# Kernel tuning notes

Hardware: AMD Instinct MI355X
Metric: run time of the kernel (lower is better)

The kernel has to match this reference:

```python
import jax, jax.numpy as jnp
import numpy as np

TEMPERATURE = 0.1
USE_RANKS = True
USE_SCORES = True
RANK_WEIGHT = 0.1
SCORE_WEIGHT = 0.01
NUM_GROUPS = 1024  # question_ids in [0, NUM_GROUPS)
BATCH = 4096
DIM = 1024


def setup_inputs() -> dict:
    key = jax.random.key(0)
    k1, k2, k3, k4, k5 = jax.random.split(key, 5)
    q_embeddings = jax.random.normal(k1, (BATCH, DIM), dtype=jnp.float32)
    a_embeddings = jax.random.normal(k2, (BATCH, DIM), dtype=jnp.float32)
    question_ids = jax.random.randint(k3, (BATCH,), 0, NUM_GROUPS, dtype=jnp.int32)
    ranks = jax.random.uniform(k4, (BATCH,), dtype=jnp.float32) * 8.0  # ordinal-ish ranks
    scores = jax.random.uniform(k5, (BATCH,), dtype=jnp.float32)
    return {
        "q_embeddings": q_embeddings,
        "a_embeddings": a_embeddings,
        "question_ids": question_ids,
        "ranks": ranks,
        "scores": scores,
    }


def _positive_weights(question_ids, ranks, scores):
    """Per-sample positive weight, normalized to sum to 1 within each question group."""
    w = jnp.ones_like(ranks)
    if USE_RANKS:
        w = w * jnp.exp(-RANK_WEIGHT * ranks)
    if USE_SCORES:
        gmax = jax.ops.segment_max(scores, question_ids, num_segments=NUM_GROUPS)
        gmin = jax.ops.segment_min(scores, question_ids, num_segments=NUM_GROUPS)
        denom = gmax[question_ids] - gmin[question_ids]
        norm = jnp.where(denom > 0, (scores - gmin[question_ids]) / jnp.where(denom > 0, denom, 1.0), 0.0)
        w = w * jnp.exp(SCORE_WEIGHT * norm)
    wsum = jax.ops.segment_sum(w, question_ids, num_segments=NUM_GROUPS)[question_ids]
    gsize = jax.ops.segment_sum(jnp.ones_like(w), question_ids, num_segments=NUM_GROUPS)[question_ids]
    w = jnp.where(wsum > 0, w / jnp.where(wsum > 0, wsum, 1.0), 1.0 / gsize)
    return w


def reference(q_embeddings, a_embeddings, question_ids, ranks, scores):
    B = q_embeddings.shape[0]
    # [B, B] similarity, one fused batched log-softmax over rows
    similarity = jnp.matmul(q_embeddings, a_embeddings.T) / TEMPERATURE
    log_probs = jax.nn.log_softmax(similarity, axis=1)
    # same-group mask: sample j is a positive for row i iff same question id
    same = (question_ids[:, None] == question_ids[None, :])
    w = _positive_weights(question_ids, ranks, scores)  # [B], group-normalized
    # loss_i = -sum_{j in group(i)} w_j * log_probs[i, j]; total averaged over batch
    per_row = -jnp.sum(jnp.where(same, w[None, :] * log_probs, 0.0), axis=1)
    loss = jnp.sum(per_row) / B
    # accuracy: argmax of each row lands inside the row's group
    pred = jnp.argmax(similarity, axis=1)
    acc = jnp.mean((question_ids[pred] == question_ids).astype(jnp.float32))
    return loss, acc
```

## Files before the change

kernel.cpp:

```cpp
#include <hip/hip_runtime.h>
#include <hip/hip_bf16.h>
#include <math.h>

#define BATCH   4096
#define DIM     1024
#define NGROUPS 1024
#define INV_T   10.0f
#define RANK_W  0.1f
#define SCORE_W 0.01f

#define BI 256
#define BJ 256
#define KC 32
#define NSTAGE (DIM/KC)
#define NFRAG_Q (BI/16)
#define NFRAG   (BI/16 + BJ/16)
#define FRAG_ELEMS 512

typedef float  floatx4 __attribute__((ext_vector_type(4)));
typedef __bf16 bf16x8  __attribute__((ext_vector_type(8)));
typedef __bf16 bf16x4  __attribute__((ext_vector_type(4)));

#define ASYNC_COPY16(gptr, lptr)                                              \
    __builtin_amdgcn_global_load_lds(                                         \
        (const __attribute__((address_space(1))) void*)(gptr),                \
        (__attribute__((address_space(3))) void*)(lptr), 16, 0, 0)


__global__ __launch_bounds__(256) void prep_kernel(
    const float* __restrict__ Q, const float* __restrict__ A,
    __bf16* __restrict__ Qp, __bf16* __restrict__ Ap,
    const int* __restrict__ qid, const float* __restrict__ ranks,
    const float* __restrict__ scores, float* __restrict__ w)
{
    const int tid = threadIdx.x;

    if (blockIdx.x >= NGROUPS) {
        __shared__ __bf16 stile[4][16 * 40];
        const int wid  = tid >> 6, lane = tid & 63;
        const int fid  = (blockIdx.x - NGROUPS) * 4 + wid;
        const int m    = fid >> 13;
        const int loc  = fid & 8191;
        const int p    = loc >> 9;
        const int t    = (loc >> 4) & 31;
        const int fi   = loc & 15;

        const float* src = (m ? A : Q);
        __bf16*      dst = (m ? Ap : Qp) + (size_t)loc * FRAG_ELEMS;

        const int r  = lane >> 2;
        const int kq = lane & 3;
        const size_t base = (size_t)(p * 256 + fi * 16 + r) * DIM + t * KC;
        const float4 v1 = *(const float4*)(src + base + kq * 4);
        const float4 v2 = *(const float4*)(src + base + 16 + kq * 4);
        bf16x4 b1, b2;
        b1[0] = (__bf16)v1.x; b1[1] = (__bf16)v1.y;
        b1[2] = (__bf16)v1.z; b1[3] = (__bf16)v1.w;
        b2[0] = (__bf16)v2.x; b2[1] = (__bf16)v2.y;
        b2[2] = (__bf16)v2.z; b2[3] = (__bf16)v2.w;

        *(bf16x4*)&stile[wid][r * 40 + kq * 4]      = b1;
        *(bf16x4*)&stile[wid][r * 40 + 16 + kq * 4] = b2;
        bf16x8 g = *(const bf16x8*)&stile[wid][(lane & 15) * 40 + (lane >> 4) * 8];
        *(bf16x8*)&dst[lane * 8] = g;
        return;
    }

    const int g = blockIdx.x, lane = tid & 63, wv = tid >> 6;
    __shared__ float rmax[4], rmin[4], rsum[4];

    float gmax = -INFINITY, gmin = INFINITY;
    for (int j = tid; j < BATCH; j += 256) {
        if (qid[j] == g) {
            float s = scores[j];
            gmax = fmaxf(gmax, s);
            gmin = fminf(gmin, s);
        }
    }
    #pragma unroll
    for (int d = 1; d < 64; d <<= 1) {
        gmax = fmaxf(gmax, __shfl_xor(gmax, d, 64));
        gmin = fminf(gmin, __shfl_xor(gmin, d, 64));
    }
    if (lane == 0) { rmax[wv] = gmax; rmin[wv] = gmin; }
    __syncthreads();
    gmax = fmaxf(fmaxf(rmax[0], rmax[1]), fmaxf(rmax[2], rmax[3]));
    gmin = fminf(fminf(rmin[0], rmin[1]), fminf(rmin[2], rmin[3]));
    const float denom     = gmax - gmin;
    const float inv_denom = (denom > 0.f) ? 1.f / denom : 0.f;

    float lsum = 0.f;
    for (int j = tid; j < BATCH; j += 256) {
        if (qid[j] == g) {
            float norm = (scores[j] - gmin) * inv_denom;
            float u = __expf(-RANK_W * ranks[j] + SCORE_W * norm);
            w[j] = u;
            lsum += u;
        }
    }
    #pragma unroll
    for (int d = 1; d < 64; d <<= 1) lsum += __shfl_xor(lsum, d, 64);
    if (lane == 0) rsum[wv] = lsum;
    __syncthreads();
    const float wsum = rsum[0] + rsum[1] + rsum[2] + rsum[3];
    const float inv  = (wsum > 0.f) ? 1.f / wsum : 0.f;
    for (int j = tid; j < BATCH; j += 256) {
        if (qid[j] == g) w[j] *= inv;
    }
}

__global__ __launch_bounds__(1024, 4) void fused_simloss_kernel(
    const __bf16* __restrict__ Qp, const __bf16* __restrict__ Ap,
    const int* __restrict__ qid, const float* __restrict__ w,
    float* __restrict__ Pm, float* __restrict__ Pl, float* __restrict__ Ps,
    float* __restrict__ Pbv, int* __restrict__ Pbi)
{
    __shared__ __bf16 sbuf[2][NFRAG * FRAG_ELEMS];

    const int bid = blockIdx.x;
    const int ib = bid >> 4, jb = bid & 15;
    const int i0 = ib * BI, j0 = jb * BJ;

    const int tid = threadIdx.x, wid = tid >> 6, lane = tid & 63;
    const int wm = wid >> 2, wn = wid & 3;
    const int quad = lane >> 4, l16 = lane & 15;

    floatx4 acc[4][4];
    #pragma unroll
    for (int m = 0; m < 4; ++m)
        #pragma unroll
        for (int n = 0; n < 4; ++n)
            #pragma unroll
            for (int c = 0; c < 4; ++c) acc[m][n][c] = 0.f;

    const __bf16* src[2];
    #pragma unroll
    for (int c = 0; c < 2; ++c) {
        const int f = wid * 2 + c;
        src[c] = (f < NFRAG_Q)
               ? Qp + ((size_t)(ib * NSTAGE * 16 + f)) * FRAG_ELEMS + lane * 8
               : Ap + ((size_t)(jb * NSTAGE * 16 + (f - NFRAG_Q))) * FRAG_ELEMS + lane * 8;
    }

    #define STAGE(buf, t)                                                     \
        do {                                                                  \
            _Pragma("unroll")                                                 \
            for (int c = 0; c < 2; ++c)                                       \
                ASYNC_COPY16(src[c] + (size_t)(t) * (16 * FRAG_ELEMS),        \
                             &sbuf[buf][(wid * 2 + c) * FRAG_ELEMS]);         \
        } while (0)

    STAGE(0, 0);

    for (int t = 0; t < NSTAGE; ++t) {
        __syncthreads();
        if (t + 1 < NSTAGE) STAGE((t + 1) & 1, t + 1);

        const __bf16* cur = sbuf[t & 1];
        bf16x8 qf[4], af[4];
        #pragma unroll
        for (int mf = 0; mf < 4; ++mf)
            qf[mf] = *(const bf16x8*)&cur[(wm * 4 + mf) * FRAG_ELEMS + lane * 8];
        #pragma unroll
        for (int nf = 0; nf < 4; ++nf)
            af[nf] = *(const bf16x8*)&cur[(NFRAG_Q + wn * 4 + nf) * FRAG_ELEMS + lane * 8];
        #pragma unroll
        for (int nf = 0; nf < 4; ++nf)
            #pragma unroll
            for (int mf = 0; mf < 4; ++mf)
                acc[mf][nf] = __builtin_amdgcn_mfma_f32_16x16x32_bf16(
                    qf[mf], af[nf], acc[mf][nf], 0, 0, 0);
    }
    #undef STAGE

    int cq[4]; float cw[4];
    #pragma unroll
    for (int n = 0; n < 4; ++n) {
        int col = j0 + wn * 64 + n * 16 + l16;
        cq[n] = qid[col];
        cw[n] = w[col];
    }
    const int slice = jb * 4 + wn;

    #pragma unroll
    for (int m = 0; m < 4; ++m) {
        #pragma unroll
        for (int reg = 0; reg < 4; ++reg) {
            const int row = i0 + wm * 64 + m * 16 + quad * 4 + reg;
            const int rq  = qid[row];

            float v[4];
            #pragma unroll
            for (int n = 0; n < 4; ++n) v[n] = acc[m][n][reg] * INV_T;

            float lm = fmaxf(fmaxf(v[0], v[1]), fmaxf(v[2], v[3]));
            float ll = __expf(v[0] - lm) + __expf(v[1] - lm) +
                       __expf(v[2] - lm) + __expf(v[3] - lm);
            float ls = 0.f;
            #pragma unroll
            for (int n = 0; n < 4; ++n) ls += (cq[n] == rq) ? cw[n] * v[n] : 0.f;

            float bv = v[0];
            int   bi = j0 + wn * 64 + l16;
            #pragma unroll
            for (int n = 1; n < 4; ++n) {
                int c = j0 + wn * 64 + n * 16 + l16;
                if (v[n] > bv) { bv = v[n]; bi = c; }
            }

            #pragma unroll
            for (int d = 1; d < 16; d <<= 1) {
                float om  = __shfl_xor(lm, d, 64);
                float ol  = __shfl_xor(ll, d, 64);
                float os  = __shfl_xor(ls, d, 64);
                float obv = __shfl_xor(bv, d, 64);
                int   obi = __shfl_xor(bi, d, 64);
                float nm = fmaxf(lm, om);
                ll = ll * __expf(lm - nm) + ol * __expf(om - nm);
                lm = nm;
                ls += os;
                if (obv > bv || (obv == bv && obi < bi)) { bv = obv; bi = obi; }
            }
            if (l16 == 0) {
                int idx = row * 64 + slice;
                Pm[idx] = lm; Pl[idx] = ll; Ps[idx] = ls;
                Pbv[idx] = bv; Pbi[idx] = bi;
            }
        }
    }
}

__global__ __launch_bounds__(256) void row_reduce_kernel(
    const float* __restrict__ Pm, const float* __restrict__ Pl,
    const float* __restrict__ Ps, const float* __restrict__ Pbv,
    const int* __restrict__ Pbi, const int* __restrict__ qid,
    float* __restrict__ pb, unsigned int* __restrict__ ticket,
    float* __restrict__ out)
{
    const int wv   = threadIdx.x >> 6;
    const int r    = blockIdx.x * 4 + wv;
    const int lane = threadIdx.x & 63;
    const int idx  = r * 64 + lane;

    float m = Pm[idx], l = Pl[idx], s = Ps[idx], bv = Pbv[idx];
    int   bi = Pbi[idx];

    #pragma unroll
    for (int d = 1; d < 64; d <<= 1) {
        float om  = __shfl_xor(m, d, 64);
        float ol  = __shfl_xor(l, d, 64);
        float os  = __shfl_xor(s, d, 64);
        float obv = __shfl_xor(bv, d, 64);
        int   obi = __shfl_xor(bi, d, 64);
        float nm = fmaxf(m, om);
        l = l * __expf(m - nm) + ol * __expf(om - nm);
        m = nm;
        s += os;
        if (obv > bv || (obv == bv && obi < bi)) { bv = obv; bi = obi; }
    }

    __shared__ float sm[4], si[4];
    __shared__ int last_flag;
    if (lane == 0) {
        sm[wv] = (m + logf(l)) - s;
        si[wv] = (qid[bi] == qid[r]) ? 1.f : 0.f;
    }
    __syncthreads();
    if (threadIdx.x == 0) {
        pb[2 * blockIdx.x]     = (sm[0] + sm[1]) + (sm[2] + sm[3]);
        pb[2 * blockIdx.x + 1] = (si[0] + si[1]) + (si[2] + si[3]);
        __threadfence();
        unsigned int my = atomicAdd(ticket, 1u);
        last_flag = (my == (BATCH / 4) - 1) ? 1 : 0;
    }
    __syncthreads();
    if (last_flag) {
        __threadfence();
        const volatile float* vpb = (const volatile float*)pb;
        float s1 = 0.f, s2 = 0.f;
        for (int i = threadIdx.x; i < BATCH / 4; i += 256) {
            s1 += vpb[2 * i];
            s2 += vpb[2 * i + 1];
        }
        #pragma unroll
        for (int d = 1; d < 64; d <<= 1) {
            s1 += __shfl_xor(s1, d, 64);
            s2 += __shfl_xor(s2, d, 64);
        }
        if (lane == 0) { sm[wv] = s1; si[wv] = s2; }
        __syncthreads();
        if (threadIdx.x == 0) {
            out[0] = ((sm[0] + sm[1]) + (sm[2] + sm[3])) * (1.f / (float)BATCH);
            out[1] = ((si[0] + si[1]) + (si[2] + si[3])) * (1.f / (float)BATCH);
        }
    }
}

extern "C" void kernel_launch(void* const* d_in, const int* in_sizes, int n_in,
                              void* d_out, int out_size, void* d_ws, size_t ws_size,
                              hipStream_t stream)
{
    const float* Q      = (const float*)d_in[0];
    const float* A      = (const float*)d_in[1];
    const int*   qid    = (const int*)d_in[2];
    const float* ranks  = (const float*)d_in[3];
    const float* scores = (const float*)d_in[4];
    float* out = (float*)d_out;

    __bf16* Qp = (__bf16*)d_ws;
    __bf16* Ap = Qp + (size_t)BATCH * DIM;
    float* w       = (float*)(Ap + (size_t)BATCH * DIM);
    float* Pm      = w + BATCH;
    float* Pl      = Pm + BATCH * 64;
    float* Ps      = Pl + BATCH * 64;
    float* Pbv     = Ps + BATCH * 64;
    int*   Pbi     = (int*)(Pbv + BATCH * 64);
    float* pb      = (float*)(Pbi + BATCH * 64);
    unsigned int* ticket = (unsigned int*)(pb + 2 * (BATCH / 4));

    hipMemsetAsync(ticket, 0, sizeof(unsigned int), stream);

    prep_kernel<<<NGROUPS + 4096, 256, 0, stream>>>(Q, A, Qp, Ap, qid, ranks, scores, w);

    fused_simloss_kernel<<<256, 1024, 0, stream>>>(Qp, Ap, qid, w, Pm, Pl, Ps, Pbv, Pbi);

    row_reduce_kernel<<<BATCH / 4, 256, 0, stream>>>(Pm, Pl, Ps, Pbv, Pbi, qid,
                                                     pb, ticket, out);
}
```

Before: 162.7 us.

## Halve row tile to 128 and fold row reduction into GEMM tail

Shrinks the GEMM block tile to 128x256 with 512 threads so 512 blocks are launched instead of 256, improving CU coverage, and repacks Q fragments in the prep kernel to match. The separate row_reduce kernel is removed. The last block to finish each row strip, found through per-strip atomic tickets, now does the row reduction, and a global ticket picks the block that writes the final output. This saves a kernel launch and better fills the GPU, at the cost of less A-tile reuse per block and a serialized tail in the last block of each strip.

```diff
diff --git a/kernel.cpp b/kernel.cpp
--- a/kernel.cpp
+++ b/kernel.cpp
@@ -9,13 +9,16 @@
 #define RANK_W  0.1f
 #define SCORE_W 0.01f
 
-#define BI 256
+#define BI 128
 #define BJ 256
 #define KC 32
 #define NSTAGE (DIM/KC)
 #define NFRAG_Q (BI/16)
-#define NFRAG   (BI/16 + BJ/16)
+#define NFRAG_A (BJ/16)
+#define NFRAG   (NFRAG_Q + NFRAG_A)
 #define FRAG_ELEMS 512
+#define GRID_I (BATCH/BI)
+#define GRID_J (BATCH/BJ)
 
 typedef float  floatx4 __attribute__((ext_vector_type(4)));
 typedef __bf16 bf16x8  __attribute__((ext_vector_type(8)));
@@ -41,16 +44,21 @@
         const int fid  = (blockIdx.x - NGROUPS) * 4 + wid;
         const int m    = fid >> 13;
         const int loc  = fid & 8191;
-        const int p    = loc >> 9;
-        const int t    = (loc >> 4) & 31;
-        const int fi   = loc & 15;
-
+
+        int row0, t;
+        if (m == 0) {
+            row0 = (loc >> 8) * 128 + (loc & 7) * 16;
+            t    = (loc >> 3) & 31;
+        } else {
+            row0 = (loc >> 9) * 256 + (loc & 15) * 16;
+            t    = (loc >> 4) & 31;
+        }
         const float* src = (m ? A : Q);
         __bf16*      dst = (m ? Ap : Qp) + (size_t)loc * FRAG_ELEMS;
 
         const int r  = lane >> 2;
         const int kq = lane & 3;
-        const size_t base = (size_t)(p * 256 + fi * 16 + r) * DIM + t * KC;
+        const size_t base = (size_t)(row0 + r) * DIM + t * KC;
         const float4 v1 = *(const float4*)(src + base + kq * 4);
         const float4 v2 = *(const float4*)(src + base + 16 + kq * 4);
         bf16x4 b1, b2;
@@ -109,11 +117,13 @@
     }
 }
 
-__global__ __launch_bounds__(1024, 4) void fused_simloss_kernel(
+__global__ __launch_bounds__(512, 4) void fused_simloss_kernel(
     const __bf16* __restrict__ Qp, const __bf16* __restrict__ Ap,
     const int* __restrict__ qid, const float* __restrict__ w,
     float* __restrict__ Pm, float* __restrict__ Pl, float* __restrict__ Ps,
-    float* __restrict__ Pbv, int* __restrict__ Pbi)
+    float* __restrict__ Pbv, int* __restrict__ Pbi,
+    float* __restrict__ pb, unsigned int* __restrict__ ticks,
+    float* __restrict__ out)
 {
     __shared__ __bf16 sbuf[2][NFRAG * FRAG_ELEMS];
 
@@ -133,21 +143,26 @@
             #pragma unroll
             for (int c = 0; c < 4; ++c) acc[m][n][c] = 0.f;
 
-    const __bf16* src[2];
-    #pragma unroll
-    for (int c = 0; c < 2; ++c) {
-        const int f = wid * 2 + c;
-        src[c] = (f < NFRAG_Q)
-               ? Qp + ((size_t)(ib * NSTAGE * 16 + f)) * FRAG_ELEMS + lane * 8
-               : Ap + ((size_t)(jb * NSTAGE * 16 + (f - NFRAG_Q))) * FRAG_ELEMS + lane * 8;
+    const __bf16* src[3];
+    int stride[3];
+    #pragma unroll
+    for (int c = 0; c < 3; ++c) {
+        const int f = wid * 3 + c;
+        if (f < NFRAG_Q) {
+            src[c]    = Qp + (size_t)(ib * 256 + f) * FRAG_ELEMS + lane * 8;
+            stride[c] = NFRAG_Q * FRAG_ELEMS;
+        } else {
+            src[c]    = Ap + (size_t)(jb * 512 + (f - NFRAG_Q)) * FRAG_ELEMS + lane * 8;
+            stride[c] = NFRAG_A * FRAG_ELEMS;
+        }
     }
 
     #define STAGE(buf, t)                                                     \
         do {                                                                  \
             _Pragma("unroll")                                                 \
-            for (int c = 0; c < 2; ++c)                                       \
-                ASYNC_COPY16(src[c] + (size_t)(t) * (16 * FRAG_ELEMS),        \
-                             &sbuf[buf][(wid * 2 + c) * FRAG_ELEMS]);         \
+            for (int c = 0; c < 3; ++c)                                       \
+                ASYNC_COPY16(src[c] + (size_t)(t) * stride[c],                \
+                             &sbuf[buf][(wid * 3 + c) * FRAG_ELEMS]);         \
         } while (0)
 
     STAGE(0, 0);
@@ -228,70 +243,64 @@
             }
         }
     }
-}
-
-__global__ __launch_bounds__(256) void row_reduce_kernel(
-    const float* __restrict__ Pm, const float* __restrict__ Pl,
-    const float* __restrict__ Ps, const float* __restrict__ Pbv,
-    const int* __restrict__ Pbi, const int* __restrict__ qid,
-    float* __restrict__ pb, unsigned int* __restrict__ ticket,
-    float* __restrict__ out)
-{
-    const int wv   = threadIdx.x >> 6;
-    const int r    = blockIdx.x * 4 + wv;
-    const int lane = threadIdx.x & 63;
-    const int idx  = r * 64 + lane;
-
-    float m = Pm[idx], l = Pl[idx], s = Ps[idx], bv = Pbv[idx];
-    int   bi = Pbi[idx];
-
-    #pragma unroll
-    for (int d = 1; d < 64; d <<= 1) {
-        float om  = __shfl_xor(m, d, 64);
-        float ol  = __shfl_xor(l, d, 64);
-        float os  = __shfl_xor(s, d, 64);
-        float obv = __shfl_xor(bv, d, 64);
-        int   obi = __shfl_xor(bi, d, 64);
-        float nm = fmaxf(m, om);
-        l = l * __expf(m - nm) + ol * __expf(om - nm);
-        m = nm;
-        s += os;
-        if (obv > bv || (obv == bv && obi < bi)) { bv = obv; bi = obi; }
-    }
-
-    __shared__ float sm[4], si[4];
-    __shared__ int last_flag;
-    if (lane == 0) {
-        sm[wv] = (m + logf(l)) - s;
-        si[wv] = (qid[bi] == qid[r]) ? 1.f : 0.f;
-    }
-    __syncthreads();
-    if (threadIdx.x == 0) {
-        pb[2 * blockIdx.x]     = (sm[0] + sm[1]) + (sm[2] + sm[3]);
-        pb[2 * blockIdx.x + 1] = (si[0] + si[1]) + (si[2] + si[3]);
+
+    __shared__ int sflag;
+    __shared__ float bm[8], ba[8];
+    __threadfence();
+    __syncthreads();
+    if (tid == 0)
+        sflag = (atomicAdd(&ticks[ib], 1u) == GRID_J - 1) ? 1 : 0;
+    __syncthreads();
+    if (!sflag) return;
+    __threadfence();
+
+    const volatile float* vPm  = (const volatile float*)Pm;
+    const volatile float* vPl  = (const volatile float*)Pl;
+    const volatile float* vPs  = (const volatile float*)Ps;
+    const volatile float* vPbv = (const volatile float*)Pbv;
+    const volatile int*   vPbi = (const volatile int*)Pbi;
+
+    float sum_loss = 0.f, sum_acc = 0.f;
+    for (int rr = wid; rr < BI; rr += 8) {
+        const int row = i0 + rr;
+        const int idx = row * 64 + lane;
+        float m  = vPm[idx], l = vPl[idx], s = vPs[idx], bv = vPbv[idx];
+        int   bi = vPbi[idx];
+        #pragma unroll
+        for (int d = 1; d < 64; d <<= 1) {
+            float om  = __shfl_xor(m, d, 64);
+            float ol  = __shfl_xor(l, d, 64);
+            float os  = __shfl_xor(s, d, 64);
+            float obv = __shfl_xor(bv, d, 64);
+            int   obi = __shfl_xor(bi, d, 64);
+            float nm = fmaxf(m, om);
+            l = l * __expf(m - nm) + ol * __expf(om - nm);
+            m = nm;
+            s += os;
+            if (obv > bv || (obv == bv && obi < bi)) { bv = obv; bi = obi; }
+        }
+        if (lane == 0) {
+            sum_loss += (m + logf(l)) - s;
+            sum_acc  += (qid[bi] == qid[row]) ? 1.f : 0.f;
+        }
+    }
+    if (lane == 0) { bm[wid] = sum_loss; ba[wid] = sum_acc; }
+    __syncthreads();
+    if (tid == 0) {
+        float t1 = 0.f, t2 = 0.f;
+        #pragma unroll
+        for (int i = 0; i < 8; ++i) { t1 += bm[i]; t2 += ba[i]; }
+        pb[2 * ib] = t1; pb[2 * ib + 1] = t2;
         __threadfence();
-        unsigned int my = atomicAdd(ticket, 1u);
-        last_flag = (my == (BATCH / 4) - 1) ? 1 : 0;
-    }
-    __syncthreads();
-    if (last_flag) {
-        __threadfence();
-        const volatile float* vpb = (const volatile float*)pb;
-        float s1 = 0.f, s2 = 0.f;
-        for (int i = threadIdx.x; i < BATCH / 4; i += 256) {
-            s1 += vpb[2 * i];
-            s2 += vpb[2 * i + 1];
-        }
-        #pragma unroll
-        for (int d = 1; d < 64; d <<= 1) {
-            s1 += __shfl_xor(s1, d, 64);
-            s2 += __shfl_xor(s2, d, 64);
-        }
-        if (lane == 0) { sm[wv] = s1; si[wv] = s2; }
-        __syncthreads();
-        if (threadIdx.x == 0) {
-            out[0] = ((sm[0] + sm[1]) + (sm[2] + sm[3])) * (1.f / (float)BATCH);
-            out[1] = ((si[0] + si[1]) + (si[2] + si[3])) * (1.f / (float)BATCH);
+        if (atomicAdd(&ticks[GRID_I], 1u) == GRID_I - 1) {
+            const volatile float* vpb = (const volatile float*)pb;
+            float s1 = 0.f, s2 = 0.f;
+            for (int i = 0; i < GRID_I; ++i) {
+                s1 += vpb[2 * i];
+                s2 += vpb[2 * i + 1];
+            }
+            out[0] = s1 * (1.f / (float)BATCH);
+            out[1] = s2 * (1.f / (float)BATCH);
         }
     }
 }
@@ -316,14 +325,12 @@
     float* Pbv     = Ps + BATCH * 64;
     int*   Pbi     = (int*)(Pbv + BATCH * 64);
     float* pb      = (float*)(Pbi + BATCH * 64);
-    unsigned int* ticket = (unsigned int*)(pb + 2 * (BATCH / 4));
-
-    hipMemsetAsync(ticket, 0, sizeof(unsigned int), stream);
+    unsigned int* ticks = (unsigned int*)(pb + 2 * GRID_I);
+
+    hipMemsetAsync(ticks, 0, (GRID_I + 1) * sizeof(unsigned int), stream);
 
     prep_kernel<<<NGROUPS + 4096, 256, 0, stream>>>(Q, A, Qp, Ap, qid, ranks, scores, w);
 
-    fused_simloss_kernel<<<256, 1024, 0, stream>>>(Qp, Ap, qid, w, Pm, Pl, Ps, Pbv, Pbi);
-
-    row_reduce_kernel<<<BATCH / 4, 256, 0, stream>>>(Pm, Pl, Ps, Pbv, Pbi, qid,
-                                                     pb, ticket, out);
+    fused_simloss_kernel<<<GRID_I * GRID_J, 512, 0, stream>>>(
+        Qp, Ap, qid, w, Pm, Pl, Ps, Pbv, Pbi, pb, ticks, out);
 }
```

Measured after the change: 322.9 us. 98.4% more time.
